# Performance work log

Hardware: AMD Instinct MI355X
Metric: run time of the kernel (lower is better)

Reference implementation:

```python
import jax, jax.numpy as jnp
import numpy as np


def _log_g(x):
    # log of g(x) = x + 0.5 for x >= 0, sigmoid(x) for x < 0
    return jnp.where(x >= 0, jnp.log(jax.nn.relu(x) + 0.5), -jax.nn.softplus(-x))


def setup_inputs() -> dict:
    key = jax.random.key(0)
    k1, k2 = jax.random.split(key)
    B, S, D = 4, 4096, 1024
    x = jax.random.normal(k1, (B, S, D), dtype=jnp.float32)
    # torch Linear(dim, 2*dim, bias=False) weight layout: [out, in]
    W = jax.random.normal(k2, (2 * D, D), dtype=jnp.float32) * (1.0 / np.sqrt(D))
    return {"x": x, "W": W}


def reference(x, W):
    # x: [B, S, D], W: [2D, D]
    hg = jnp.einsum('bsd,ed->bse', x, W)            # [B, S, 2D]
    hidden, gate = jnp.split(hg, 2, axis=-1)        # each [B, S, D]

    log_coeffs = -jax.nn.softplus(gate)             # log(1 - sigmoid(gate))
    log_z = -jax.nn.softplus(-gate)                 # log(sigmoid(gate))
    log_values = log_z + _log_g(hidden)

    # Heinsen associative scan in log space over the sequence axis
    a_star = jnp.cumsum(log_coeffs, axis=1)
    log_h = a_star + jax.lax.cumlogsumexp(log_values - a_star, axis=1)
    out = jnp.exp(log_h)                            # [B, S, D]; to_out is Identity
    return out
```

## Files before the change

kernel.cpp:

```cpp
#include <hip/hip_runtime.h>
#include <hip/hip_bf16.h>
#include <hip/hip_fp16.h>
#include <cstdint>

typedef unsigned short us;
typedef us   us8 __attribute__((ext_vector_type(8)));
typedef short s8v __attribute__((ext_vector_type(8)));
typedef float f4v __attribute__((ext_vector_type(4)));
typedef __fp16 pk2 __attribute__((ext_vector_type(2)));

#define BB 4
#define SS 4096
#define DD 1024
#define MM (BB * SS)
#define NN (2 * DD)
#define KK DD

#define BM 128
#define BN 128
#define BK 64

#define CHUNK 32
#define NC (SS / CHUNK)
#define BDD (BB * DD)
#define DQ (DD / 4)

__device__ inline us f2bf(float f) {
  unsigned u = __float_as_uint(f);
  u += 0x7fffu + ((u >> 16) & 1u);
  return (us)(u >> 16);
}

__global__ __launch_bounds__(256) void cvt_both(const float* __restrict__ x,
                                                const float* __restrict__ W,
                                                us* __restrict__ xb,
                                                us* __restrict__ wb,
                                                long nx) {
  long i = ((long)blockIdx.x * 256 + threadIdx.x) * 8;
  const float* in;
  us* out;
  if (i < nx) { in = x + i; out = xb + i; }
  else        { in = W + (i - nx); out = wb + (i - nx); }
  const float4* p = (const float4*)in;
  float4 a = p[0], b = p[1];
  us8 o;
  o[0] = f2bf(a.x); o[1] = f2bf(a.y); o[2] = f2bf(a.z); o[3] = f2bf(a.w);
  o[4] = f2bf(b.x); o[5] = f2bf(b.y); o[6] = f2bf(b.z); o[7] = f2bf(b.w);
  *(us8*)out = o;
}

#define GLD16(g, l)                                                        \
  __builtin_amdgcn_global_load_lds(                                        \
      (const __attribute__((address_space(1))) void*)(g),                  \
      (__attribute__((address_space(3))) void*)(l), 16, 0, 0)

__device__ inline void gate_cv(float hid, float gat, float& coef, float& v) {
  float e = __expf(gat);
  coef = __builtin_amdgcn_rcpf(1.0f + e);
  float z = 1.0f - coef;
  float eh = __expf(hid < 0.0f ? hid : 0.0f);
  float gneg = eh * __builtin_amdgcn_rcpf(1.0f + eh);
  float g = (hid >= 0.0f) ? (hid + 0.5f) : gneg;
  v = z * g;
}

__global__ __launch_bounds__(256) void gemm_fused(const us* __restrict__ A,
                                                  const us* __restrict__ B,
                                                  unsigned* __restrict__ cv,
                                                  float* __restrict__ cp,
                                                  float* __restrict__ ch) {
  __shared__ __align__(16) us smem[BM * BK + BN * BK];
  us* As = smem;
  us* Bs = smem + BM * BK;
  unsigned* T = (unsigned*)smem;

  const int tid  = threadIdx.x;
  const int lane = tid & 63;
  const int w    = tid >> 6;
  const int wm   = w & 1;
  const int wn   = w >> 1;
  const long bm  = (long)blockIdx.x * BM;
  const int  d0  = blockIdx.y * 64;

  const int srow = lane >> 3;
  const int sseg = (lane & 7) ^ srow;

  const int fr = lane & 15;
  const int fq = lane >> 4;

  int aoff[4][2], boff[4][2];
#pragma unroll
  for (int mt = 0; mt < 4; ++mt) {
    int row = wm * 64 + mt * 16 + fr;
#pragma unroll
    for (int kk = 0; kk < 2; ++kk) {
      int seg = kk * 4 + fq;
      aoff[mt][kk] = row * BK + ((seg ^ (row & 7)) * 8);
    }
  }
#pragma unroll
  for (int nt = 0; nt < 4; ++nt) {
    int row = wn * 64 + nt * 16 + fr;
#pragma unroll
    for (int kk = 0; kk < 2; ++kk) {
      int seg = kk * 4 + fq;
      boff[nt][kk] = row * BK + ((seg ^ (row & 7)) * 8);
    }
  }

  f4v acc[4][4] = {};

  const us* Ap[4];
  const us* Bp[4];
#pragma unroll
  for (int i = 0; i < 4; ++i) {
    int lr = w * 32 + i * 8 + srow;
    Ap[i] = A + (bm + lr) * (long)KK + sseg * 8;
    int wrow = d0 + ((lr >> 5) << 4) + (lr & 15) + (((lr >> 4) & 1) << 10);
    Bp[i] = B + (long)wrow * KK + sseg * 8;
  }

  for (int kt = 0; kt < KK / BK; ++kt) {
    __syncthreads();
#pragma unroll
    for (int i = 0; i < 4; ++i) {
      GLD16(Ap[i], &As[(w * 32 + i * 8) * BK]);
      GLD16(Bp[i], &Bs[(w * 32 + i * 8) * BK]);
      Ap[i] += BK;
      Bp[i] += BK;
    }
    __syncthreads();

#pragma unroll
    for (int kk = 0; kk < 2; ++kk) {
      s8v af[4], bf[4];
#pragma unroll
      for (int mt = 0; mt < 4; ++mt) af[mt] = *(const s8v*)&As[aoff[mt][kk]];
#pragma unroll
      for (int nt = 0; nt < 4; ++nt) bf[nt] = *(const s8v*)&Bs[boff[nt][kk]];
#pragma unroll
      for (int mt = 0; mt < 4; ++mt)
#pragma unroll
        for (int nt = 0; nt < 4; ++nt)
          acc[mt][nt] = __builtin_amdgcn_mfma_f32_16x16x32_bf16(
              af[mt], bf[nt], acc[mt][nt], 0, 0, 0);
    }
  }

  __syncthreads();
#pragma unroll
  for (int mt = 0; mt < 4; ++mt) {
    int lr0 = wm * 64 + mt * 16 + fq * 4;
#pragma unroll
    for (int p = 0; p < 2; ++p) {
      int ld = (wn * 2 + p) * 16 + fr;
      f4v hv = acc[mt][2 * p];
      f4v gv = acc[mt][2 * p + 1];
#pragma unroll
      for (int r = 0; r < 4; ++r) {
        float coef, v;
        gate_cv(hv[r], gv[r], coef, v);
        pk2 pk = __builtin_amdgcn_cvt_pkrtz(coef, v);
        T[(lr0 + r) * 64 + ld] = __builtin_bit_cast(unsigned, pk);
      }
    }
  }
  __syncthreads();

#pragma unroll
  for (int j = 0; j < 8; ++j) {
    int chunk = j * 256 + tid;
    int row = chunk >> 4;
    int q   = chunk & 15;
    uint4 val = *(const uint4*)&T[row * 64 + q * 4];
    *(uint4*)(cv + (size_t)(bm + row) * DD + d0 + q * 4) = val;
  }

  {
    const int d = tid & 63;
    const int c = tid >> 6;
    float P = 1.0f, h = 0.0f;
#pragma unroll
    for (int i = 0; i < CHUNK; ++i) {
      unsigned u = T[(c * CHUNK + i) * 64 + d];
      __half2 hv = *(__half2*)&u;
      float cf = __half2float(hv.x);
      h = fmaf(cf, h, __half2float(hv.y));
      P *= cf;
    }
    const int b  = (int)(bm / SS);
    const int cg = (int)((bm % SS) / CHUNK) + c;
    const int idx = cg * BDD + b * DD + d0 + d;
    cp[idx] = P;
    ch[idx] = h;
  }
}

__global__ __launch_bounds__(256) void scan_pass2(const float* __restrict__ cp,
                                                  const float* __restrict__ ch,
                                                  float* __restrict__ carry) {
  const int bd = blockIdx.x * 256 + threadIdx.x;
  float h = 0.0f;
  for (int cb = 0; cb < NC; cb += 16) {
    float p[16], v[16];
#pragma unroll
    for (int i = 0; i < 16; ++i) {
      p[i] = cp[(cb + i) * BDD + bd];
      v[i] = ch[(cb + i) * BDD + bd];
    }
#pragma unroll
    for (int i = 0; i < 16; ++i) {
      carry[(cb + i) * BDD + bd] = h;
      h = fmaf(p[i], h, v[i]);
    }
  }
}

__global__ __launch_bounds__(256) void scan_pass3(const uint4* __restrict__ cv,
                                                  const float* __restrict__ carry,
                                                  float4* __restrict__ out) {
  const int q = threadIdx.x;
  const int c = blockIdx.y;
  const int b = blockIdx.z;
  const size_t rbase = ((size_t)b * SS + (size_t)c * CHUNK) * DQ + q;
  const uint4* base = cv + rbase;
  float4* obase = out + rbase;
  float4 h = *(const float4*)&carry[c * BDD + b * DD + 4 * q];
#pragma unroll 4
  for (int t = 0; t < CHUNK; ++t) {
    uint4 u = base[(size_t)t * DQ];
    __half2 a0 = *(__half2*)&u.x;
    __half2 a1 = *(__half2*)&u.y;
    __half2 a2 = *(__half2*)&u.z;
    __half2 a3 = *(__half2*)&u.w;
    h.x = fmaf(__half2float(a0.x), h.x, __half2float(a0.y));
    h.y = fmaf(__half2float(a1.x), h.y, __half2float(a1.y));
    h.z = fmaf(__half2float(a2.x), h.z, __half2float(a2.y));
    h.w = fmaf(__half2float(a3.x), h.w, __half2float(a3.y));
    obase[(size_t)t * DQ] = h;
  }
}

extern "C" void kernel_launch(void* const* d_in, const int* in_sizes, int n_in,
                              void* d_out, int out_size, void* d_ws, size_t ws_size,
                              hipStream_t stream) {
  const float* x = (const float*)d_in[0];
  const float* W = (const float*)d_in[1];
  float4* out = (float4*)d_out;

  const long nx = (long)MM * KK;
  const long nw = (long)NN * KK;

  char* ws = (char*)d_ws;
  unsigned* cv = (unsigned*)ws;      ws += (size_t)MM * DD * sizeof(unsigned);
  us* xb = (us*)ws;                  ws += (size_t)nx * sizeof(us);
  us* wb = (us*)ws;                  ws += (size_t)nw * sizeof(us);
  float* cp = (float*)ws;            ws += (size_t)NC * BDD * sizeof(float);
  float* chh = (float*)ws;           ws += (size_t)NC * BDD * sizeof(float);
  float* carry = (float*)ws;         ws += (size_t)NC * BDD * sizeof(float);

  cvt_both<<<(int)((nx + nw) / 8 / 256), 256, 0, stream>>>(x, W, xb, wb, nx);

  gemm_fused<<<dim3(MM / BM, DD / 64), 256, 0, stream>>>(xb, wb, cv, cp, chh);

  scan_pass2<<<dim3(BDD / 256), 256, 0, stream>>>(cp, chh, carry);
  scan_pass3<<<dim3(1, NC, BB), 256, 0, stream>>>((const uint4*)cv, carry, out);
}
```

Measured before the change: 228.0 us.

## Fold chunk-carry scan into pass3 by recomputing prefix per block

Removes the separate scan_pass2 kernel and its carry buffer. Each pass3 block now recomputes its incoming carry by serially combining the chunk summaries (P, h) of all preceding chunks for its batch and feature slice. This saves one launch and the sequential 128-step carry pass with its carry writes and reads. The cost is redundant work that grows with chunk index, up to 127 steps of float4 loads per thread and about 64 on average, added in front of each block's own scan.

```diff
diff --git a/kernel.cpp b/kernel.cpp
--- a/kernel.cpp
+++ b/kernel.cpp
@@ -196,36 +196,45 @@
   }
 }
 
-__global__ __launch_bounds__(256) void scan_pass2(const float* __restrict__ cp,
+__global__ __launch_bounds__(256) void scan_pass3(const uint4* __restrict__ cv,
+                                                  const float* __restrict__ cp,
                                                   const float* __restrict__ ch,
-                                                  float* __restrict__ carry) {
-  const int bd = blockIdx.x * 256 + threadIdx.x;
-  float h = 0.0f;
-  for (int cb = 0; cb < NC; cb += 16) {
-    float p[16], v[16];
-#pragma unroll
-    for (int i = 0; i < 16; ++i) {
-      p[i] = cp[(cb + i) * BDD + bd];
-      v[i] = ch[(cb + i) * BDD + bd];
-    }
-#pragma unroll
-    for (int i = 0; i < 16; ++i) {
-      carry[(cb + i) * BDD + bd] = h;
-      h = fmaf(p[i], h, v[i]);
-    }
-  }
-}
-
-__global__ __launch_bounds__(256) void scan_pass3(const uint4* __restrict__ cv,
-                                                  const float* __restrict__ carry,
                                                   float4* __restrict__ out) {
   const int q = threadIdx.x;
   const int c = blockIdx.y;
   const int b = blockIdx.z;
+
+  const float4* cpb = (const float4*)(cp + (size_t)b * DD) + q;
+  const float4* chb = (const float4*)(ch + (size_t)b * DD) + q;
+  float4 h = make_float4(0.0f, 0.0f, 0.0f, 0.0f);
+  int cc = 0;
+  for (; cc + 8 <= c; cc += 8) {
+    float4 p4[8], v4[8];
+#pragma unroll
+    for (int i = 0; i < 8; ++i) {
+      p4[i] = cpb[(size_t)(cc + i) * (BDD / 4)];
+      v4[i] = chb[(size_t)(cc + i) * (BDD / 4)];
+    }
+#pragma unroll
+    for (int i = 0; i < 8; ++i) {
+      h.x = fmaf(p4[i].x, h.x, v4[i].x);
+      h.y = fmaf(p4[i].y, h.y, v4[i].y);
+      h.z = fmaf(p4[i].z, h.z, v4[i].z);
+      h.w = fmaf(p4[i].w, h.w, v4[i].w);
+    }
+  }
+  for (; cc < c; ++cc) {
+    float4 p4 = cpb[(size_t)cc * (BDD / 4)];
+    float4 v4 = chb[(size_t)cc * (BDD / 4)];
+    h.x = fmaf(p4.x, h.x, v4.x);
+    h.y = fmaf(p4.y, h.y, v4.y);
+    h.z = fmaf(p4.z, h.z, v4.z);
+    h.w = fmaf(p4.w, h.w, v4.w);
+  }
+
   const size_t rbase = ((size_t)b * SS + (size_t)c * CHUNK) * DQ + q;
   const uint4* base = cv + rbase;
   float4* obase = out + rbase;
-  float4 h = *(const float4*)&carry[c * BDD + b * DD + 4 * q];
 #pragma unroll 4
   for (int t = 0; t < CHUNK; ++t) {
     uint4 u = base[(size_t)t * DQ];
@@ -257,12 +266,10 @@
   us* wb = (us*)ws;                  ws += (size_t)nw * sizeof(us);
   float* cp = (float*)ws;            ws += (size_t)NC * BDD * sizeof(float);
   float* chh = (float*)ws;           ws += (size_t)NC * BDD * sizeof(float);
-  float* carry = (float*)ws;         ws += (size_t)NC * BDD * sizeof(float);
 
   cvt_both<<<(int)((nx + nw) / 8 / 256), 256, 0, stream>>>(x, W, xb, wb, nx);
 
   gemm_fused<<<dim3(MM / BM, DD / 64), 256, 0, stream>>>(xb, wb, cv, cp, chh);
 
-  scan_pass2<<<dim3(BDD / 256), 256, 0, stream>>>(cp, chh, carry);
-  scan_pass3<<<dim3(1, NC, BB), 256, 0, stream>>>((const uint4*)cv, carry, out);
-}
+  scan_pass3<<<dim3(1, NC, BB), 256, 0, stream>>>((const uint4*)cv, cp, chh, out);
+}
```

After: 234.8 us. 3.0% more time.

## Enlarge GEMM tile to 256x256 with double-buffered LDS and interleaved loads

Applied to the files above, without the earlier changes.

Grows the fused GEMM tile from 128x128 to 256x256 on 512 threads (8 waves). It double-buffers LDS across two K-steps and spreads global-to-LDS loads across eight MFMA phases, using explicit vmcnt waits, barriers and s_setprio. The aim is to raise arithmetic intensity and overlap memory traffic with matrix math instead of synchronising around every K-step. The epilogue and chunk-scan summaries are widened to the 128-column output slice. In exchange it uses 128KB of LDS, more accumulator registers and hand-managed waitcnt ordering, which is fragile.

```diff
diff --git a/kernel.cpp b/kernel.cpp
--- a/kernel.cpp
+++ b/kernel.cpp
@@ -16,8 +16,8 @@
 #define NN (2 * DD)
 #define KK DD
 
-#define BM 128
-#define BN 128
+#define BM 256
+#define BN 256
 #define BK 64
 
 #define CHUNK 32
@@ -64,14 +64,16 @@
   v = z * g;
 }
 
-__global__ __launch_bounds__(256) void gemm_fused(const us* __restrict__ A,
-                                                  const us* __restrict__ B,
-                                                  unsigned* __restrict__ cv,
-                                                  float* __restrict__ cp,
-                                                  float* __restrict__ ch) {
-  __shared__ __align__(16) us smem[BM * BK + BN * BK];
-  us* As = smem;
-  us* Bs = smem + BM * BK;
+__global__ __launch_bounds__(512, 2) void gemm_fused(const us* __restrict__ A,
+                                                     const us* __restrict__ Bw,
+                                                     unsigned* __restrict__ cv,
+                                                     float* __restrict__ cp,
+                                                     float* __restrict__ ch) {
+  __shared__ __align__(16) us smem[4 * 256 * 64];
+  us* As0 = smem;
+  us* Bs0 = smem + 256 * 64;
+  us* As1 = smem + 2 * 256 * 64;
+  us* Bs1 = smem + 3 * 256 * 64;
   unsigned* T = (unsigned*)smem;
 
   const int tid  = threadIdx.x;
@@ -80,119 +82,143 @@
   const int wm   = w & 1;
   const int wn   = w >> 1;
   const long bm  = (long)blockIdx.x * BM;
-  const int  d0  = blockIdx.y * 64;
+  const int  d0  = blockIdx.y * 128;
 
   const int srow = lane >> 3;
   const int sseg = (lane & 7) ^ srow;
 
   const int fr = lane & 15;
   const int fq = lane >> 4;
-
-  int aoff[4][2], boff[4][2];
-#pragma unroll
-  for (int mt = 0; mt < 4; ++mt) {
-    int row = wm * 64 + mt * 16 + fr;
-#pragma unroll
-    for (int kk = 0; kk < 2; ++kk) {
-      int seg = kk * 4 + fq;
-      aoff[mt][kk] = row * BK + ((seg ^ (row & 7)) * 8);
-    }
-  }
-#pragma unroll
-  for (int nt = 0; nt < 4; ++nt) {
-    int row = wn * 64 + nt * 16 + fr;
-#pragma unroll
-    for (int kk = 0; kk < 2; ++kk) {
-      int seg = kk * 4 + fq;
-      boff[nt][kk] = row * BK + ((seg ^ (row & 7)) * 8);
-    }
-  }
-
-  f4v acc[4][4] = {};
-
-  const us* Ap[4];
-  const us* Bp[4];
-#pragma unroll
-  for (int i = 0; i < 4; ++i) {
-    int lr = w * 32 + i * 8 + srow;
-    Ap[i] = A + (bm + lr) * (long)KK + sseg * 8;
+  const int f7 = fr & 7;
+
+  const int a_r0 = ((w >> 2) * 128) + ((w & 3) * 16);
+  const int b_r0 = w * 16;
+
+  const us* Abase = A + (bm + srow) * (long)KK + sseg * 8;
+
+  auto stA = [&](int r0, int kt, us* dst) {
+    GLD16(Abase + (long)r0 * KK + kt * 64, dst + r0 * 64);
+  };
+  auto stB = [&](int r0, int kt, us* dst) {
+    int lr = r0 + srow;
     int wrow = d0 + ((lr >> 5) << 4) + (lr & 15) + (((lr >> 4) & 1) << 10);
-    Bp[i] = B + (long)wrow * KK + sseg * 8;
-  }
-
-  for (int kt = 0; kt < KK / BK; ++kt) {
-    __syncthreads();
-#pragma unroll
-    for (int i = 0; i < 4; ++i) {
-      GLD16(Ap[i], &As[(w * 32 + i * 8) * BK]);
-      GLD16(Bp[i], &Bs[(w * 32 + i * 8) * BK]);
-      Ap[i] += BK;
-      Bp[i] += BK;
-    }
-    __syncthreads();
-
-#pragma unroll
-    for (int kk = 0; kk < 2; ++kk) {
-      s8v af[4], bf[4];
-#pragma unroll
-      for (int mt = 0; mt < 4; ++mt) af[mt] = *(const s8v*)&As[aoff[mt][kk]];
-#pragma unroll
-      for (int nt = 0; nt < 4; ++nt) bf[nt] = *(const s8v*)&Bs[boff[nt][kk]];
-#pragma unroll
-      for (int mt = 0; mt < 4; ++mt)
+    GLD16(Bw + (long)wrow * KK + kt * 64 + sseg * 8, dst + r0 * 64);
+  };
+
+  f4v acc[8][4] = {};
+
+  stA(a_r0, 0, As0);       stA(a_r0 + 8, 0, As0);
+  stA(a_r0 + 64, 0, As0);  stA(a_r0 + 72, 0, As0);
+  stB(b_r0, 0, Bs0);       stB(b_r0 + 8, 0, Bs0);
+  stB(b_r0 + 128, 0, Bs0); stB(b_r0 + 136, 0, Bs0);
+  stB(b_r0, 1, Bs1);       stB(b_r0 + 8, 1, Bs1);
+  stB(b_r0 + 128, 1, Bs1); stB(b_r0 + 136, 1, Bs1);
+  stA(a_r0, 1, As1);       stA(a_r0 + 8, 1, As1);
+  asm volatile("s_waitcnt vmcnt(6)" ::: "memory");
+  __builtin_amdgcn_s_barrier();
+
+  s8v bf[4][2];
+  for (int it = 0; it < 8; ++it) {
+    const int t1 = 2 * it + 1;
+    const int s0 = (it < 7) ? (2 * it + 2) : 14;
+    const int s1 = (it < 7) ? (2 * it + 3) : 15;
+#pragma unroll
+    for (int p = 0; p < 8; ++p) {
+      const int q = p & 3;
+      const us* Asb = (p < 4) ? As0 : As1;
+      const us* Bsb = (p < 4) ? Bs0 : Bs1;
+      if (q == 0) {
 #pragma unroll
         for (int nt = 0; nt < 4; ++nt)
-          acc[mt][nt] = __builtin_amdgcn_mfma_f32_16x16x32_bf16(
-              af[mt], bf[nt], acc[mt][nt], 0, 0, 0);
-    }
-  }
-
-  __syncthreads();
-#pragma unroll
-  for (int mt = 0; mt < 4; ++mt) {
-    int lr0 = wm * 64 + mt * 16 + fq * 4;
-#pragma unroll
-    for (int p = 0; p < 2; ++p) {
-      int ld = (wn * 2 + p) * 16 + fr;
-      f4v hv = acc[mt][2 * p];
-      f4v gv = acc[mt][2 * p + 1];
+#pragma unroll
+          for (int kk = 0; kk < 2; ++kk)
+            bf[nt][kk] = *(const s8v*)&Bsb[(wn * 64 + nt * 16 + fr) * 64 +
+                                           (((kk * 4 + fq) ^ f7) * 8)];
+      }
+      s8v af[2][2];
+#pragma unroll
+      for (int m2 = 0; m2 < 2; ++m2)
+#pragma unroll
+        for (int kk = 0; kk < 2; ++kk)
+          af[m2][kk] = *(const s8v*)&Asb[(wm * 128 + (2 * q + m2) * 16 + fr) * 64 +
+                                         (((kk * 4 + fq) ^ f7) * 8)];
+      if (p == 0)      { stA(a_r0 + 64, t1, As1); stA(a_r0 + 72, t1, As1); }
+      else if (p == 1) { stB(b_r0, s0, Bs0);       stB(b_r0 + 8, s0, Bs0); }
+      else if (p == 2) { stB(b_r0 + 128, s0, Bs0); stB(b_r0 + 136, s0, Bs0); }
+      else if (p == 3) { stA(a_r0, s0, As0);       stA(a_r0 + 8, s0, As0);
+                         asm volatile("s_waitcnt vmcnt(6)" ::: "memory"); }
+      else if (p == 4) { stA(a_r0 + 64, s0, As0);  stA(a_r0 + 72, s0, As0); }
+      else if (p == 5) { stB(b_r0, s1, Bs1);       stB(b_r0 + 8, s1, Bs1); }
+      else if (p == 6) { stB(b_r0 + 128, s1, Bs1); stB(b_r0 + 136, s1, Bs1); }
+      else             { stA(a_r0, s1, As1);       stA(a_r0 + 8, s1, As1);
+                         asm volatile("s_waitcnt vmcnt(6)" ::: "memory"); }
+      __builtin_amdgcn_s_barrier();
+      asm volatile("s_waitcnt lgkmcnt(0)" ::: "memory");
+      __builtin_amdgcn_s_setprio(1);
+#pragma unroll
+      for (int kk = 0; kk < 2; ++kk)
+#pragma unroll
+        for (int m2 = 0; m2 < 2; ++m2)
+#pragma unroll
+          for (int nt = 0; nt < 4; ++nt)
+            acc[2 * q + m2][nt] = __builtin_amdgcn_mfma_f32_16x16x32_bf16(
+                af[m2][kk], bf[nt][kk], acc[2 * q + m2][nt], 0, 0, 0);
+      __builtin_amdgcn_s_setprio(0);
+      __builtin_amdgcn_s_barrier();
+    }
+  }
+
+  asm volatile("s_waitcnt vmcnt(0)" ::: "memory");
+  __builtin_amdgcn_s_barrier();
+#pragma unroll
+  for (int mt = 0; mt < 8; ++mt) {
+    int lr0 = wm * 128 + mt * 16 + fq * 4;
+#pragma unroll
+    for (int pp = 0; pp < 2; ++pp) {
+      int ld = (wn * 2 + pp) * 16 + fr;
+      f4v hv = acc[mt][2 * pp];
+      f4v gv = acc[mt][2 * pp + 1];
 #pragma unroll
       for (int r = 0; r < 4; ++r) {
         float coef, v;
         gate_cv(hv[r], gv[r], coef, v);
         pk2 pk = __builtin_amdgcn_cvt_pkrtz(coef, v);
-        T[(lr0 + r) * 64 + ld] = __builtin_bit_cast(unsigned, pk);
+        T[(lr0 + r) * 128 + ld] = __builtin_bit_cast(unsigned, pk);
       }
     }
   }
   __syncthreads();
 
 #pragma unroll
-  for (int j = 0; j < 8; ++j) {
-    int chunk = j * 256 + tid;
-    int row = chunk >> 4;
-    int q   = chunk & 15;
-    uint4 val = *(const uint4*)&T[row * 64 + q * 4];
-    *(uint4*)(cv + (size_t)(bm + row) * DD + d0 + q * 4) = val;
+  for (int j = 0; j < 16; ++j) {
+    int chunk = j * 512 + tid;
+    int row = chunk >> 5;
+    int qq  = chunk & 31;
+    uint4 val = *(const uint4*)&T[row * 128 + qq * 4];
+    *(uint4*)(cv + (size_t)(bm + row) * DD + d0 + qq * 4) = val;
   }
 
   {
-    const int d = tid & 63;
-    const int c = tid >> 6;
-    float P = 1.0f, h = 0.0f;
-#pragma unroll
-    for (int i = 0; i < CHUNK; ++i) {
-      unsigned u = T[(c * CHUNK + i) * 64 + d];
-      __half2 hv = *(__half2*)&u;
-      float cf = __half2float(hv.x);
-      h = fmaf(cf, h, __half2float(hv.y));
-      P *= cf;
-    }
+    const int d  = tid & 127;
+    const int c0 = tid >> 7;
     const int b  = (int)(bm / SS);
-    const int cg = (int)((bm % SS) / CHUNK) + c;
-    const int idx = cg * BDD + b * DD + d0 + d;
-    cp[idx] = P;
-    ch[idx] = h;
+    const int cg0 = (int)((bm % SS) / CHUNK);
+#pragma unroll
+    for (int half = 0; half < 2; ++half) {
+      const int c = c0 + half * 4;
+      float P = 1.0f, h = 0.0f;
+#pragma unroll
+      for (int i2 = 0; i2 < CHUNK; ++i2) {
+        unsigned u = T[(c * CHUNK + i2) * 128 + d];
+        __half2 hv2 = *(__half2*)&u;
+        float cf = __half2float(hv2.x);
+        h = fmaf(cf, h, __half2float(hv2.y));
+        P *= cf;
+      }
+      const int idx = (cg0 + c) * BDD + b * DD + d0 + d;
+      cp[idx] = P;
+      ch[idx] = h;
+    }
   }
 }
 
@@ -261,7 +287,7 @@
 
   cvt_both<<<(int)((nx + nw) / 8 / 256), 256, 0, stream>>>(x, W, xb, wb, nx);
 
-  gemm_fused<<<dim3(MM / BM, DD / 64), 256, 0, stream>>>(xb, wb, cv, cp, chh);
+  gemm_fused<<<dim3(MM / BM, NN / BN), 512, 0, stream>>>(xb, wb, cv, cp, chh);
 
   scan_pass2<<<dim3(BDD / 256), 256, 0, stream>>>(cp, chh, carry);
   scan_pass3<<<dim3(1, NC, BB), 256, 0, stream>>>((const uint4*)cv, carry, out);
```

Result: slower. 236.2 us (+3.6%).
